# Kernel tuning notes

Hardware: AMD Instinct MI355X
Metric: run time of the kernel (lower is better)

Reference implementation:

```python
import jax, jax.numpy as jnp
import numpy as np

H = 128  # hidden width of the PINN MLP


def _mlp_scalar(pt, W0, b0, W1, b1, W2, b2, W3, b3):
    # pt: [2] -> scalar u(x, y); tanh MLP as used in PINN solid-mechanics nets
    h = jnp.tanh(pt @ W0 + b0)
    h = jnp.tanh(h @ W1 + b1)
    h = jnp.tanh(h @ W2 + b2)
    return (h @ W3 + b3)[0]


def setup_inputs() -> dict:
    key = jax.random.key(0)
    ks = jax.random.split(key, 6)
    N = 131072
    # Xavier-ish scaling so tanh stays in its smooth regime
    X = jax.random.normal(ks[0], (N, 2), dtype=jnp.float32)
    W0 = jax.random.normal(ks[1], (2, H), dtype=jnp.float32) * (1.0 / np.sqrt(2.0))
    b0 = jnp.zeros((H,), dtype=jnp.float32)
    W1 = jax.random.normal(ks[2], (H, H), dtype=jnp.float32) * (1.0 / np.sqrt(H))
    b1 = jnp.zeros((H,), dtype=jnp.float32)
    W2 = jax.random.normal(ks[3], (H, H), dtype=jnp.float32) * (1.0 / np.sqrt(H))
    b2 = jnp.zeros((H,), dtype=jnp.float32)
    W3 = jax.random.normal(ks[4], (H, 1), dtype=jnp.float32) * (1.0 / np.sqrt(H))
    b3 = jnp.zeros((1,), dtype=jnp.float32)
    return {"X": X, "W0": W0, "b0": b0, "W1": W1, "b1": b1,
            "W2": W2, "b2": b2, "W3": W3, "b3": b3}


def reference(X, W0, b0, W1, b1, W2, b2, W3, b3):
    # Per-point Hessian of u w.r.t. (x, y). Each collocation point is
    # independent, so TF's batched gradient-of-sum equals the per-point
    # derivative; forward-over-reverse (jacfwd o jacrev) vmapped over N is
    # the efficient fused form of the two nested GradientTapes.
    f = lambda pt: _mlp_scalar(pt, W0, b0, W1, b1, W2, b2, W3, b3)
    hess = jax.vmap(jax.jacfwd(jax.jacrev(f)))(X)  # [N, 2, 2]
    du_dxx = hess[:, 0, 0][:, None]  # [N, 1]
    du_dxy = hess[:, 0, 1][:, None]  # [N, 1]
    du_dyy = hess[:, 1, 1][:, None]  # [N, 1]
    return (du_dxx, du_dxy, du_dyy)
```

## Files before the change

### kernel.cpp

```cpp
#include <hip/hip_runtime.h>

#define H    128
#define P    32
#define NT   768
#define WSTR 40

typedef _Float16 v8h __attribute__((ext_vector_type(8)));
typedef __fp16   h2  __attribute__((ext_vector_type(2)));
typedef float    v4f __attribute__((ext_vector_type(4)));

union PK4 { h2 h[4]; uint4 u; };
union PK2 { h2 h[2]; uint2 u; };

__device__ __forceinline__ int soct(int pl, int p, int o) {
    return ((pl * P + p) * 16 + (o ^ (p & 15))) << 3;
}

__global__ void wt_convert(const float* __restrict__ W1,
                           const float* __restrict__ W2,
                           _Float16* __restrict__ ws) {
    __shared__ float tile[32][33];
    const int b  = blockIdx.x;
    const int l  = b >> 4;
    const int t  = b & 15;
    const int kt = t >> 2, jt = t & 3;
    const float* __restrict__ W = l ? W2 : W1;
    const int tr = threadIdx.x >> 5;
    const int tc = threadIdx.x & 31;
    #pragma unroll
    for (int s = 0; s < 4; ++s)
        tile[tr + s * 8][tc] = W[(kt * 32 + tr + s * 8) * H + jt * 32 + tc];
    __syncthreads();
    #pragma unroll
    for (int s = 0; s < 4; ++s)
        ws[l * H * H + (jt * 32 + tr + s * 8) * H + kt * 32 + tc] =
            (_Float16)tile[tc][tr + s * 8];
}

__device__ __forceinline__ void tanh_d2(float z, float& a, float& g1, float& g2) {
    const float e = __expf(2.f * z);
    a  = 1.f - 2.f / (e + 1.f);
    g1 = 1.f - a * a;
    g2 = -2.f * a * g1;
}

__global__ __launch_bounds__(NT, 6)
void pinn_hess_mfma(const float* __restrict__ X,
                    const float* __restrict__ W0, const float* __restrict__ b0,
                    const _Float16* __restrict__ Wt,
                    const float* __restrict__ b1, const float* __restrict__ b2,
                    const float* __restrict__ W3,
                    float* __restrict__ out, int N)
{
    __shared__ _Float16 sS[6 * P * H];
    __shared__ _Float16 sW[2][H * WSTR];

    const int tid   = threadIdx.x;
    const int wave  = tid >> 6;
    const int plane = wave >> 1;
    const int mhalf = wave & 1;
    const int lane  = tid & 63;
    const int quad  = lane >> 4;
    const int l15   = lane & 15;
    const int pbase = blockIdx.x * P;

    for (int i = tid; i < P * 16; i += NT) {
        const int p = i >> 4, o = i & 15;
        const float x = X[2 * (pbase + p)];
        const float y = X[2 * (pbase + p) + 1];
        float wxv[8], wyv[8], bv[8];
        *(float4*)&wxv[0] = *(const float4*)&W0[o * 8];
        *(float4*)&wxv[4] = *(const float4*)&W0[o * 8 + 4];
        *(float4*)&wyv[0] = *(const float4*)&W0[H + o * 8];
        *(float4*)&wyv[4] = *(const float4*)&W0[H + o * 8 + 4];
        *(float4*)&bv[0]  = *(const float4*)&b0[o * 8];
        *(float4*)&bv[4]  = *(const float4*)&b0[o * 8 + 4];
        float r[6][8];
        #pragma unroll
        for (int u = 0; u < 8; ++u) {
            float a, g1, g2;
            tanh_d2(fmaf(x, wxv[u], fmaf(y, wyv[u], bv[u])), a, g1, g2);
            r[0][u] = a;
            r[1][u] = g1 * wxv[u];
            r[2][u] = g1 * wyv[u];
            r[3][u] = g2 * wxv[u] * wxv[u];
            r[4][u] = g2 * wxv[u] * wyv[u];
            r[5][u] = g2 * wyv[u] * wyv[u];
        }
        #pragma unroll
        for (int pl = 0; pl < 6; ++pl) {
            PK4 q;
            #pragma unroll
            for (int h = 0; h < 4; ++h)
                q.h[h] = __builtin_amdgcn_cvt_pkrtz(r[pl][2*h], r[pl][2*h+1]);
            *(uint4*)&sS[soct(pl, p, o)] = q.u;
        }
    }

    for (int layer = 0; layer < 2; ++layer) {
        const _Float16* __restrict__ Wg = Wt + layer * H * H;

        auto stage = [&](int kc, int buf) {
            for (int c = tid; c < 512; c += NT) {
                const int j = c >> 2, o = c & 3;
                *(v8h*)&sW[buf][j * WSTR + o * 8] =
                    *(const v8h*)&Wg[j * H + kc * 32 + o * 8];
            }
        };

        stage(0, 0);
        __syncthreads();

        v4f C[4][2];
        #pragma unroll
        for (int m = 0; m < 4; ++m) { C[m][0] = (v4f){0,0,0,0}; C[m][1] = (v4f){0,0,0,0}; }

        for (int kc = 0; kc < 4; ++kc) {
            const int buf = kc & 1;
            if (kc < 3) stage(kc + 1, buf ^ 1);
            const v8h B0 = *(const v8h*)&sS[soct(plane, l15,      kc * 4 + quad)];
            const v8h B1 = *(const v8h*)&sS[soct(plane, 16 + l15, kc * 4 + quad)];
            #pragma unroll
            for (int m = 0; m < 4; ++m) {
                const int mt = mhalf * 4 + m;
                const v8h A = *(const v8h*)&sW[buf][(mt * 16 + l15) * WSTR + quad * 8];
                C[m][0] = __builtin_amdgcn_mfma_f32_16x16x32_f16(A, B0, C[m][0], 0, 0, 0);
                C[m][1] = __builtin_amdgcn_mfma_f32_16x16x32_f16(A, B1, C[m][1], 0, 0, 0);
            }
            if (kc == 3) {
                #pragma unroll
                for (int m = 0; m < 4; ++m)
                    #pragma unroll
                    for (int nt = 0; nt < 2; ++nt) {
                        PK2 q;
                        q.h[0] = __builtin_amdgcn_cvt_pkrtz(C[m][nt][0], C[m][nt][1]);
                        q.h[1] = __builtin_amdgcn_cvt_pkrtz(C[m][nt][2], C[m][nt][3]);
                        const int mt = mhalf * 4 + m;
                        const int p = nt * 16 + l15;
                        const int o = mt * 2 + (quad >> 1);
                        *(uint2*)&sS[soct(plane, p, o) + (quad & 1) * 4] = q.u;
                    }
            }
            __syncthreads();
        }

        if (layer == 0) {
            for (int i = tid; i < P * 16; i += NT) {
                const int p = i >> 4, o = i & 15;
                const int base = soct(0, p, o);
                v8h zp[6];
                #pragma unroll
                for (int pl = 0; pl < 6; ++pl)
                    zp[pl] = *(const v8h*)&sS[base + pl * 4096];
                float bv[8];
                *(float4*)&bv[0] = *(const float4*)&b1[o * 8];
                *(float4*)&bv[4] = *(const float4*)&b1[o * 8 + 4];
                float r[6][8];
                #pragma unroll
                for (int u = 0; u < 8; ++u) {
                    float a, g1, g2;
                    tanh_d2((float)zp[0][u] + bv[u], a, g1, g2);
                    const float tx = (float)zp[1][u], ty = (float)zp[2][u];
                    r[0][u] = a;
                    r[1][u] = g1 * tx;
                    r[2][u] = g1 * ty;
                    r[3][u] = fmaf(g2 * tx, tx, g1 * (float)zp[3][u]);
                    r[4][u] = fmaf(g2 * tx, ty, g1 * (float)zp[4][u]);
                    r[5][u] = fmaf(g2 * ty, ty, g1 * (float)zp[5][u]);
                }
                #pragma unroll
                for (int pl = 0; pl < 6; ++pl) {
                    PK4 q;
                    #pragma unroll
                    for (int h = 0; h < 4; ++h)
                        q.h[h] = __builtin_amdgcn_cvt_pkrtz(r[pl][2*h], r[pl][2*h+1]);
                    *(uint4*)&sS[base + pl * 4096] = q.u;
                }
            }
        } else {
            if (tid < 512) {
                const int p = tid >> 4, o = tid & 15;
                float oxx = 0.f, oxy = 0.f, oyy = 0.f;
                const int base = soct(0, p, o);
                v8h zp[6];
                #pragma unroll
                for (int pl = 0; pl < 6; ++pl)
                    zp[pl] = *(const v8h*)&sS[base + pl * 4096];
                float bv[8], w3v[8];
                *(float4*)&bv[0]  = *(const float4*)&b2[o * 8];
                *(float4*)&bv[4]  = *(const float4*)&b2[o * 8 + 4];
                *(float4*)&w3v[0] = *(const float4*)&W3[o * 8];
                *(float4*)&w3v[4] = *(const float4*)&W3[o * 8 + 4];
                #pragma unroll
                for (int u = 0; u < 8; ++u) {
                    float a, g1, g2;
                    tanh_d2((float)zp[0][u] + bv[u], a, g1, g2);
                    const float tx = (float)zp[1][u], ty = (float)zp[2][u];
                    oxx = fmaf(w3v[u], fmaf(g2 * tx, tx, g1 * (float)zp[3][u]), oxx);
                    oxy = fmaf(w3v[u], fmaf(g2 * tx, ty, g1 * (float)zp[4][u]), oxy);
                    oyy = fmaf(w3v[u], fmaf(g2 * ty, ty, g1 * (float)zp[5][u]), oyy);
                }
                #pragma unroll
                for (int off = 8; off > 0; off >>= 1) {
                    oxx += __shfl_down(oxx, off, 16);
                    oxy += __shfl_down(oxy, off, 16);
                    oyy += __shfl_down(oyy, off, 16);
                }
                if (o == 0) {
                    out[pbase + p]         = oxx;
                    out[N + pbase + p]     = oxy;
                    out[2 * N + pbase + p] = oyy;
                }
            }
        }
    }
}

extern "C" void kernel_launch(void* const* d_in, const int* in_sizes, int n_in,
                              void* d_out, int out_size, void* d_ws, size_t ws_size,
                              hipStream_t stream) {
    const float* X  = (const float*)d_in[0];
    const float* W0 = (const float*)d_in[1];
    const float* b0 = (const float*)d_in[2];
    const float* W1 = (const float*)d_in[3];
    const float* b1 = (const float*)d_in[4];
    const float* W2 = (const float*)d_in[5];
    const float* b2 = (const float*)d_in[6];
    const float* W3 = (const float*)d_in[7];

    const int N = in_sizes[0] / 2;
    float* out = (float*)d_out;
    _Float16* ws = (_Float16*)d_ws;

    hipLaunchKernelGGL(wt_convert, dim3(32), dim3(256), 0, stream, W1, W2, ws);

    hipLaunchKernelGGL(pinn_hess_mfma, dim3(N / P), dim3(NT), 0, stream,
                       X, W0, b0, ws, b1, b2, W3, out, N);
}
```

Measured before the change: 164.6 us.

## Swap MFMA operand roles so each wave covers all six planes and fuse epilogue in registers

The block drops from 12 to 8 waves. Each wave now computes all six derivative planes for half the points and a 32-column slice of outputs, so one weight fragment is reused across the six planes. The tanh/derivative epilogue now reads the MFMA accumulators directly instead of writing fp16 results to shared memory and reading them back. The final layer reduces across the four column slices through shared memory. The weight-conversion kernel is simplified to a packed per-thread transpose. The change trades fewer waves per block and more accumulator registers for less shared-memory round-tripping. It also adds scattered 2-byte shared stores in the layer-0 epilogue.

After: 156.8 us. 4.7% less time.

```diff
diff --git a/kernel.cpp b/kernel.cpp
--- a/kernel.cpp
+++ b/kernel.cpp
@@ -2,7 +2,7 @@
 
 #define H    128
 #define P    32
-#define NT   768
+#define NT   512
 #define WSTR 40
 
 typedef _Float16 v8h __attribute__((ext_vector_type(8)));
@@ -10,7 +10,6 @@
 typedef float    v4f __attribute__((ext_vector_type(4)));
 
 union PK4 { h2 h[4]; uint4 u; };
-union PK2 { h2 h[2]; uint2 u; };
 
 __device__ __forceinline__ int soct(int pl, int p, int o) {
     return ((pl * P + p) * 16 + (o ^ (p & 15))) << 3;
@@ -19,22 +18,16 @@
 __global__ void wt_convert(const float* __restrict__ W1,
                            const float* __restrict__ W2,
                            _Float16* __restrict__ ws) {
-    __shared__ float tile[32][33];
-    const int b  = blockIdx.x;
-    const int l  = b >> 4;
-    const int t  = b & 15;
-    const int kt = t >> 2, jt = t & 3;
+    const int t = blockIdx.x * 64 + threadIdx.x;
+    const int l = t >> 13;
+    const int r = t & 8191;
+    const int j = r >> 6, kp = r & 63;
     const float* __restrict__ W = l ? W2 : W1;
-    const int tr = threadIdx.x >> 5;
-    const int tc = threadIdx.x & 31;
-    #pragma unroll
-    for (int s = 0; s < 4; ++s)
-        tile[tr + s * 8][tc] = W[(kt * 32 + tr + s * 8) * H + jt * 32 + tc];
-    __syncthreads();
-    #pragma unroll
-    for (int s = 0; s < 4; ++s)
-        ws[l * H * H + (jt * 32 + tr + s * 8) * H + kt * 32 + tc] =
-            (_Float16)tile[tc][tr + s * 8];
+    const float a = W[(2 * kp) * H + j];
+    const float b = W[(2 * kp + 1) * H + j];
+    union { h2 h; unsigned u; } q;
+    q.h = __builtin_amdgcn_cvt_pkrtz(a, b);
+    ((unsigned*)ws)[t] = q.u;
 }
 
 __device__ __forceinline__ void tanh_d2(float z, float& a, float& g1, float& g2) {
@@ -44,7 +37,7 @@
     g2 = -2.f * a * g1;
 }
 
-__global__ __launch_bounds__(NT, 6)
+__global__ __launch_bounds__(NT, 4)
 void pinn_hess_mfma(const float* __restrict__ X,
                     const float* __restrict__ W0, const float* __restrict__ b0,
                     const _Float16* __restrict__ Wt,
@@ -57,15 +50,15 @@
 
     const int tid   = threadIdx.x;
     const int wave  = tid >> 6;
-    const int plane = wave >> 1;
-    const int mhalf = wave & 1;
+    const int phalf = wave & 1;
+    const int jpair = wave >> 1;
     const int lane  = tid & 63;
     const int quad  = lane >> 4;
     const int l15   = lane & 15;
     const int pbase = blockIdx.x * P;
 
-    for (int i = tid; i < P * 16; i += NT) {
-        const int p = i >> 4, o = i & 15;
+    {
+        const int p = tid >> 4, o = tid & 15;
         const float x = X[2 * (pbase + p)];
         const float y = X[2 * (pbase + p) + 1];
         float wxv[8], wyv[8], bv[8];
@@ -101,116 +94,95 @@
         const _Float16* __restrict__ Wg = Wt + layer * H * H;
 
         auto stage = [&](int kc, int buf) {
-            for (int c = tid; c < 512; c += NT) {
-                const int j = c >> 2, o = c & 3;
-                *(v8h*)&sW[buf][j * WSTR + o * 8] =
-                    *(const v8h*)&Wg[j * H + kc * 32 + o * 8];
-            }
+            const int j = tid >> 2, o = tid & 3;
+            *(v8h*)&sW[buf][j * WSTR + o * 8] =
+                *(const v8h*)&Wg[j * H + kc * 32 + o * 8];
         };
 
         stage(0, 0);
         __syncthreads();
 
-        v4f C[4][2];
+        v4f C[6][2];
         #pragma unroll
-        for (int m = 0; m < 4; ++m) { C[m][0] = (v4f){0,0,0,0}; C[m][1] = (v4f){0,0,0,0}; }
+        for (int pl = 0; pl < 6; ++pl) { C[pl][0] = (v4f){0,0,0,0}; C[pl][1] = (v4f){0,0,0,0}; }
 
         for (int kc = 0; kc < 4; ++kc) {
             const int buf = kc & 1;
             if (kc < 3) stage(kc + 1, buf ^ 1);
-            const v8h B0 = *(const v8h*)&sS[soct(plane, l15,      kc * 4 + quad)];
-            const v8h B1 = *(const v8h*)&sS[soct(plane, 16 + l15, kc * 4 + quad)];
-            #pragma unroll
-            for (int m = 0; m < 4; ++m) {
-                const int mt = mhalf * 4 + m;
-                const v8h A = *(const v8h*)&sW[buf][(mt * 16 + l15) * WSTR + quad * 8];
-                C[m][0] = __builtin_amdgcn_mfma_f32_16x16x32_f16(A, B0, C[m][0], 0, 0, 0);
-                C[m][1] = __builtin_amdgcn_mfma_f32_16x16x32_f16(A, B1, C[m][1], 0, 0, 0);
-            }
-            if (kc == 3) {
-                #pragma unroll
-                for (int m = 0; m < 4; ++m)
-                    #pragma unroll
-                    for (int nt = 0; nt < 2; ++nt) {
-                        PK2 q;
-                        q.h[0] = __builtin_amdgcn_cvt_pkrtz(C[m][nt][0], C[m][nt][1]);
-                        q.h[1] = __builtin_amdgcn_cvt_pkrtz(C[m][nt][2], C[m][nt][3]);
-                        const int mt = mhalf * 4 + m;
-                        const int p = nt * 16 + l15;
-                        const int o = mt * 2 + (quad >> 1);
-                        *(uint2*)&sS[soct(plane, p, o) + (quad & 1) * 4] = q.u;
-                    }
+            const v8h B0 = *(const v8h*)&sW[buf][(jpair * 32 + l15)      * WSTR + quad * 8];
+            const v8h B1 = *(const v8h*)&sW[buf][(jpair * 32 + 16 + l15) * WSTR + quad * 8];
+            #pragma unroll
+            for (int pl = 0; pl < 6; ++pl) {
+                const v8h A = *(const v8h*)&sS[soct(pl, phalf * 16 + l15, kc * 4 + quad)];
+                C[pl][0] = __builtin_amdgcn_mfma_f32_16x16x32_f16(A, B0, C[pl][0], 0, 0, 0);
+                C[pl][1] = __builtin_amdgcn_mfma_f32_16x16x32_f16(A, B1, C[pl][1], 0, 0, 0);
             }
             __syncthreads();
         }
 
         if (layer == 0) {
-            for (int i = tid; i < P * 16; i += NT) {
-                const int p = i >> 4, o = i & 15;
-                const int base = soct(0, p, o);
-                v8h zp[6];
-                #pragma unroll
-                for (int pl = 0; pl < 6; ++pl)
-                    zp[pl] = *(const v8h*)&sS[base + pl * 4096];
-                float bv[8];
-                *(float4*)&bv[0] = *(const float4*)&b1[o * 8];
-                *(float4*)&bv[4] = *(const float4*)&b1[o * 8 + 4];
-                float r[6][8];
-                #pragma unroll
-                for (int u = 0; u < 8; ++u) {
+            #pragma unroll
+            for (int nt = 0; nt < 2; ++nt) {
+                const int j  = jpair * 32 + nt * 16 + l15;
+                const int ob = j >> 3, wi = j & 7;
+                const float bb = b1[j];
+                #pragma unroll
+                for (int r = 0; r < 4; ++r) {
+                    const int p = phalf * 16 + quad * 4 + r;
                     float a, g1, g2;
-                    tanh_d2((float)zp[0][u] + bv[u], a, g1, g2);
-                    const float tx = (float)zp[1][u], ty = (float)zp[2][u];
-                    r[0][u] = a;
-                    r[1][u] = g1 * tx;
-                    r[2][u] = g1 * ty;
-                    r[3][u] = fmaf(g2 * tx, tx, g1 * (float)zp[3][u]);
-                    r[4][u] = fmaf(g2 * tx, ty, g1 * (float)zp[4][u]);
-                    r[5][u] = fmaf(g2 * ty, ty, g1 * (float)zp[5][u]);
-                }
-                #pragma unroll
-                for (int pl = 0; pl < 6; ++pl) {
-                    PK4 q;
-                    #pragma unroll
-                    for (int h = 0; h < 4; ++h)
-                        q.h[h] = __builtin_amdgcn_cvt_pkrtz(r[pl][2*h], r[pl][2*h+1]);
-                    *(uint4*)&sS[base + pl * 4096] = q.u;
+                    tanh_d2(C[0][nt][r] + bb, a, g1, g2);
+                    const float tx = C[1][nt][r], ty = C[2][nt][r];
+                    sS[soct(0, p, ob) + wi] = (_Float16)a;
+                    sS[soct(1, p, ob) + wi] = (_Float16)(g1 * tx);
+                    sS[soct(2, p, ob) + wi] = (_Float16)(g1 * ty);
+                    sS[soct(3, p, ob) + wi] = (_Float16)fmaf(g2 * tx, tx, g1 * C[3][nt][r]);
+                    sS[soct(4, p, ob) + wi] = (_Float16)fmaf(g2 * tx, ty, g1 * C[4][nt][r]);
+                    sS[soct(5, p, ob) + wi] = (_Float16)fmaf(g2 * ty, ty, g1 * C[5][nt][r]);
                 }
             }
         } else {
-            if (tid < 512) {
-                const int p = tid >> 4, o = tid & 15;
-                float oxx = 0.f, oxy = 0.f, oyy = 0.f;
-                const int base = soct(0, p, o);
-                v8h zp[6];
-                #pragma unroll
-                for (int pl = 0; pl < 6; ++pl)
-                    zp[pl] = *(const v8h*)&sS[base + pl * 4096];
-                float bv[8], w3v[8];
-                *(float4*)&bv[0]  = *(const float4*)&b2[o * 8];
-                *(float4*)&bv[4]  = *(const float4*)&b2[o * 8 + 4];
-                *(float4*)&w3v[0] = *(const float4*)&W3[o * 8];
-                *(float4*)&w3v[4] = *(const float4*)&W3[o * 8 + 4];
-                #pragma unroll
-                for (int u = 0; u < 8; ++u) {
+            float hxx[4] = {0,0,0,0}, hxy[4] = {0,0,0,0}, hyy[4] = {0,0,0,0};
+            #pragma unroll
+            for (int nt = 0; nt < 2; ++nt) {
+                const int j = jpair * 32 + nt * 16 + l15;
+                const float bb = b2[j];
+                const float w3 = W3[j];
+                #pragma unroll
+                for (int r = 0; r < 4; ++r) {
                     float a, g1, g2;
-                    tanh_d2((float)zp[0][u] + bv[u], a, g1, g2);
-                    const float tx = (float)zp[1][u], ty = (float)zp[2][u];
-                    oxx = fmaf(w3v[u], fmaf(g2 * tx, tx, g1 * (float)zp[3][u]), oxx);
-                    oxy = fmaf(w3v[u], fmaf(g2 * tx, ty, g1 * (float)zp[4][u]), oxy);
-                    oyy = fmaf(w3v[u], fmaf(g2 * ty, ty, g1 * (float)zp[5][u]), oyy);
-                }
-                #pragma unroll
-                for (int off = 8; off > 0; off >>= 1) {
-                    oxx += __shfl_down(oxx, off, 16);
-                    oxy += __shfl_down(oxy, off, 16);
-                    oyy += __shfl_down(oyy, off, 16);
-                }
-                if (o == 0) {
-                    out[pbase + p]         = oxx;
-                    out[N + pbase + p]     = oxy;
-                    out[2 * N + pbase + p] = oyy;
-                }
+                    tanh_d2(C[0][nt][r] + bb, a, g1, g2);
+                    const float tx = C[1][nt][r], ty = C[2][nt][r];
+                    hxx[r] = fmaf(w3, fmaf(g2 * tx, tx, g1 * C[3][nt][r]), hxx[r]);
+                    hxy[r] = fmaf(w3, fmaf(g2 * tx, ty, g1 * C[4][nt][r]), hxy[r]);
+                    hyy[r] = fmaf(w3, fmaf(g2 * ty, ty, g1 * C[5][nt][r]), hyy[r]);
+                }
+            }
+            #pragma unroll
+            for (int off = 8; off > 0; off >>= 1)
+                #pragma unroll
+                for (int r = 0; r < 4; ++r) {
+                    hxx[r] += __shfl_down(hxx[r], off, 16);
+                    hxy[r] += __shfl_down(hxy[r], off, 16);
+                    hyy[r] += __shfl_down(hyy[r], off, 16);
+                }
+            float* sRed = (float*)&sW[0][0];
+            if (l15 == 0) {
+                #pragma unroll
+                for (int r = 0; r < 4; ++r) {
+                    const int p = phalf * 16 + quad * 4 + r;
+                    sRed[0 * 128 + jpair * 32 + p] = hxx[r];
+                    sRed[1 * 128 + jpair * 32 + p] = hxy[r];
+                    sRed[2 * 128 + jpair * 32 + p] = hyy[r];
+                }
+            }
+            __syncthreads();
+            if (tid < 96) {
+                const int c = tid >> 5, p = tid & 31;
+                float acc = 0.f;
+                #pragma unroll
+                for (int jp = 0; jp < 4; ++jp)
+                    acc += sRed[c * 128 + jp * 32 + p];
+                out[c * N + pbase + p] = acc;
             }
         }
     }
@@ -232,7 +204,7 @@
     float* out = (float*)d_out;
     _Float16* ws = (_Float16*)d_ws;
 
-    hipLaunchKernelGGL(wt_convert, dim3(32), dim3(256), 0, stream, W1, W2, ws);
+    hipLaunchKernelGGL(wt_convert, dim3(256), dim3(64), 0, stream, W1, W2, ws);
 
     hipLaunchKernelGGL(pinn_hess_mfma, dim3(N / P), dim3(NT), 0, stream,
                        X, W0, b0, ws, b1, b2, W3, out, N);
```
